# Kernel optimization log

Measured on AMD Instinct MI355X. Metric: run time of the kernel, lower is better.

## Reference

```python
import jax, jax.numpy as jnp
import numpy as np

N, D, OUT, E, K = 65536, 256, 256, 8, 2  # tokens, input_dim, output_dim, num_experts, top-k


def setup_inputs() -> dict:
    key = jax.random.key(0)
    k1, k2, k3, k4 = jax.random.split(key, 4)
    x = jax.random.normal(k1, (N, D), dtype=jnp.float32)
    # xavier_normal-like init for the gate
    w_gate = jax.random.normal(k2, (D, E), dtype=jnp.float32) * np.float32(np.sqrt(2.0 / (D + E)))
    # PWLayer params stacked over experts: bias init zeros, weight std 0.02
    expert_bias = jax.random.normal(k3, (E, D), dtype=jnp.float32) * 0.01
    expert_weight = jax.random.normal(k4, (E, OUT, D), dtype=jnp.float32) * 0.02
    return {"x": x, "w_gate": w_gate, "expert_bias": expert_bias, "expert_weight": expert_weight}


def reference(x, w_gate, expert_bias, expert_weight):
    # --- noisy_top_k_gating (eval mode: clean logits only) ---
    logits = x @ w_gate                                   # [N, E]
    top_v, top_i = jax.lax.top_k(logits, K)               # [N, K]
    sparse_logits = jnp.full_like(logits, -jnp.inf)
    rows = jnp.arange(logits.shape[0])[:, None]           # [N, 1]
    sparse_logits = sparse_logits.at[rows, top_i].set(top_v)
    gates = jax.nn.softmax(sparse_logits, axis=-1)        # [N, E], zeros off the top-k
    # --- dense all-expert PWLayer pass: (x - bias_e) @ W_e^T ---
    centered = x[:, None, :] - expert_bias[None, :, :]    # [N, E, D]
    expert_stack = jnp.einsum('ned,eod->neo', centered, expert_weight)  # [N, E, OUT]
    # --- gated combine ---
    return jnp.einsum('ne,neo->no', gates, expert_stack)  # [N, OUT]
```

## Files before the change

kernel.cpp:

```cpp
#include <hip/hip_runtime.h>
#include <hip/hip_bf16.h>
#include <math.h>

#define N_TOK 65536
#define DIM   256
#define NEXP  8

using frag_ab = __attribute__((ext_vector_type(8))) short;
using frag_cd = __attribute__((ext_vector_type(4))) float;

__device__ __forceinline__ unsigned short f2bf(float f) {
  unsigned u = __float_as_uint(f);
  u += 0x7FFFu + ((u >> 16) & 1u);
  return (unsigned short)(u >> 16);
}

__device__ __forceinline__ void gl2lds16(const unsigned short* g, unsigned short* l) {
  __builtin_amdgcn_global_load_lds(
      (const __attribute__((address_space(1))) void*)g,
      (__attribute__((address_space(3))) void*)l, 16, 0, 0);
}


__global__ __launch_bounds__(256) void k_prep(
    const float* __restrict__ w,
    const float* __restrict__ bias,
    unsigned short* __restrict__ Wb,
    float* __restrict__ c,
    int* __restrict__ meta) {
  int tid = threadIdx.x;
  int wid = (blockIdx.x * 256 + tid) >> 6;
  int lane = tid & 63;
  int e = wid >> 8, o = wid & 255;
  const float* wr = w + (size_t)(e * 256 + o) * DIM + lane * 4;
  float4 wv = *(const float4*)wr;
  const float* br = bias + e * DIM + lane * 4;
  float4 bv = *(const float4*)br;
  float s = wv.x * bv.x + wv.y * bv.y + wv.z * bv.z + wv.w * bv.w;
  #pragma unroll
  for (int m = 1; m < 64; m <<= 1) s += __shfl_xor(s, m, 64);
  if (lane == 0) c[e * 256 + o] = s;
  ushort4 h; h.x = f2bf(wv.x); h.y = f2bf(wv.y); h.z = f2bf(wv.z); h.w = f2bf(wv.w);
  *(ushort4*)(Wb + (size_t)e * 65536 + (size_t)(lane >> 1) * 2048 + o * 8 + (lane & 1) * 4) = h;
  if (blockIdx.x == 0 && tid < 192) meta[tid] = 0;
}

__global__ __launch_bounds__(256) void k_gating(
    const float* __restrict__ x,
    const float* __restrict__ wg,
    unsigned short* __restrict__ xb,
    int* __restrict__ routeE,
    float* __restrict__ routeG,
    int* __restrict__ meta) {
  __shared__ double swg[DIM * NEXP];
  __shared__ float  chunk[128 * 33];
  __shared__ double sPar[128 * NEXP];
  __shared__ int    hcnt[64];
  int tid = threadIdx.x;
  int tok0 = blockIdx.x * 128;
  int sub = tid >> 7, tk = tid & 127;

  for (int i = tid; i < DIM * NEXP; i += 256) swg[i] = (double)wg[i];
  if (tid < 64) hcnt[tid] = 0;

  double p[NEXP];
  #pragma unroll
  for (int e = 0; e < NEXP; e++) p[e] = 0.0;

  for (int dc = 0; dc < 8; dc++) {
    __syncthreads();
    #pragma unroll
    for (int i = 0; i < 4; i++) {
      int f = i * 256 + tid;
      int r = f >> 3, c4 = (f & 7) * 4;
      const float4 v = *(const float4*)(x + (size_t)(tok0 + r) * DIM + dc * 32 + c4);
      ushort4 h; h.x = f2bf(v.x); h.y = f2bf(v.y); h.z = f2bf(v.z); h.w = f2bf(v.w);
      *(ushort4*)(xb + (size_t)(tok0 + r) * DIM + dc * 32 + c4) = h;
      float* dst = &chunk[r * 33 + c4];
      dst[0] = v.x; dst[1] = v.y; dst[2] = v.z; dst[3] = v.w;
    }
    __syncthreads();
    if ((dc >> 2) == sub) {
      #pragma unroll 8
      for (int cc = 0; cc < 32; cc++) {
        double xv = (double)chunk[tk * 33 + cc];
        const double* wrow = &swg[(dc * 32 + cc) * NEXP];
        #pragma unroll
        for (int e = 0; e < NEXP; e++) p[e] += xv * wrow[e];
      }
    }
  }

  if (sub == 1) {
    #pragma unroll
    for (int e = 0; e < NEXP; e++) sPar[tk * NEXP + e] = p[e];
  }
  __syncthreads();
  if (sub == 0) {
    #pragma unroll
    for (int e = 0; e < NEXP; e++) p[e] += sPar[tk * NEXP + e];

    int i1 = 0; double v1 = p[0];
    #pragma unroll
    for (int e = 1; e < NEXP; e++) { if (p[e] > v1) { v1 = p[e]; i1 = e; } }
    int i2 = -1; double v2 = -1e300;
    #pragma unroll
    for (int e = 0; e < NEXP; e++) { if (e != i1 && p[e] > v2) { v2 = p[e]; i2 = e; } }
    double t = exp(v2 - v1);
    float g1 = (float)(1.0 / (1.0 + t));
    float g2 = 1.0f - g1;

    int n = tok0 + tk;
    routeE[n] = i1 | (i2 << 8);
    *(float2*)(routeG + 2 * (size_t)n) = make_float2(g1, g2);
    int a = i1 < i2 ? i1 : i2, b = i1 < i2 ? i2 : i1;
    atomicAdd(&hcnt[a * 8 + b], 1);
  }
  __syncthreads();
  if (tid < 64) atomicAdd(&meta[tid], hcnt[tid]);
}

__global__ void k_scan(int* __restrict__ meta) {
  if (threadIdx.x == 0) {
    int run = 0;
    for (int p = 0; p < 64; p++) {
      meta[64 + p] = run; meta[128 + p] = run;
      run += ((meta[p] + 127) >> 7) << 7;
    }
  }
}

__global__ __launch_bounds__(1024) void k_scatter(
    const int* __restrict__ routeE, const float* __restrict__ routeG,
    int* __restrict__ meta,
    int* __restrict__ srcTok, float* __restrict__ srcGA, float* __restrict__ srcGB) {
  __shared__ int cnt[64], bse[64];
  int tid = threadIdx.x;
  if (tid < 64) cnt[tid] = 0;
  __syncthreads();
  int n = blockIdx.x * 1024 + tid;
  int ep = routeE[n];
  int e1 = ep & 255, e2 = ep >> 8;
  float2 g = *(const float2*)(routeG + 2 * (size_t)n);
  int a = e1 < e2 ? e1 : e2, b = e1 < e2 ? e2 : e1;
  float ga = e1 < e2 ? g.x : g.y;
  float gb = e1 < e2 ? g.y : g.x;
  int pid = a * 8 + b;
  int r = atomicAdd(&cnt[pid], 1);
  __syncthreads();
  if (tid < 64) bse[tid] = atomicAdd(&meta[128 + tid], cnt[tid]);
  __syncthreads();
  int p = bse[pid] + r;
  srcTok[p] = n; srcGA[p] = ga; srcGB[p] = gb;
}

__global__ __launch_bounds__(512, 2) void k_gemm_pair(
    const unsigned short* __restrict__ xb,
    const unsigned short* __restrict__ Wb,
    const int* __restrict__ meta,
    const int* __restrict__ srcTok,
    const float* __restrict__ srcGA, const float* __restrict__ srcGB,
    const float* __restrict__ c,
    float* __restrict__ out) {
  __shared__ unsigned short sA[4][128 * 64];
  __shared__ int   sTok[128];
  __shared__ float sGAs[128], sGBs[128];
  __shared__ float sCorA[256], sCorB[256];
  int tid = threadIdx.x;

  int rem = blockIdx.x, pid = 0, ne = 0;
  for (pid = 0; pid < 64; pid++) {
    ne = meta[pid];
    int tiles = (ne + 127) >> 7;
    if (rem < tiles) break;
    rem -= tiles;
  }
  if (pid == 64) return;
  int ea = pid >> 3, eb = pid & 7;
  int mt = rem;
  int slot0 = meta[64 + pid] + mt * 128;

  if (tid < 128) {
    int idx = mt * 128 + tid;
    bool v = idx < ne;
    sTok[tid]  = v ? srcTok[slot0 + tid] : 0;
    sGAs[tid]  = v ? srcGA[slot0 + tid] : 0.f;
    sGBs[tid]  = v ? srcGB[slot0 + tid] : 1.f;
  } else if (tid < 192) {
    ((float4*)sCorA)[tid - 128] = ((const float4*)(c + ea * 256))[tid - 128];
  } else if (tid < 256) {
    ((float4*)sCorB)[tid - 192] = ((const float4*)(c + eb * 256))[tid - 192];
  }
  __syncthreads();

  int w = tid >> 6, lane = tid & 63;
  int lrow = lane >> 3, lchk = lane & 7;

  #pragma unroll
  for (int q = 0; q < 2; q++) {
    int r0 = w * 16 + q * 8;
    int r  = r0 + lrow;
    int cc = (lchk - r) & 7;
    const unsigned short* src = xb + (size_t)sTok[r] * 256 + cc * 8;
    #pragma unroll
    for (int kk = 0; kk < 4; kk++)
      gl2lds16(src + kk * 64, &sA[kk][r0 * 64]);
  }
  __syncthreads();

  int wm = w & 1, wn = w >> 1;
  int lr = lane & 15, lk = lane >> 4;
  int offA[2][4];
  #pragma unroll
  for (int ks = 0; ks < 2; ks++)
    #pragma unroll
    for (int i = 0; i < 4; i++) {
      int ra = wm * 64 + i * 16 + lr;
      offA[ks][i] = ra * 64 + ((ks * 4 + lk + ra) & 7) * 8;
    }

  const unsigned short* bBaseA =
      Wb + (size_t)ea * 65536 + (size_t)lk * 2048 + (wn * 64 + lr) * 8;
  const unsigned short* bBaseB =
      Wb + (size_t)eb * 65536 + (size_t)lk * 2048 + (wn * 64 + lr) * 8;

  frag_cd acc[4][4];
  #pragma unroll
  for (int i = 0; i < 4; i++)
    #pragma unroll
    for (int j = 0; j < 4; j++)
      acc[i][j] = (frag_cd){0.f, 0.f, 0.f, 0.f};

#define PHASE(BB) do {                                                      \
    _Pragma("unroll")                                                       \
    for (int kk = 0; kk < 4; kk++) {                                        \
      _Pragma("unroll")                                                     \
      for (int ks = 0; ks < 2; ks++) {                                      \
        frag_ab av[4], bv[4];                                               \
        _Pragma("unroll")                                                   \
        for (int j = 0; j < 4; j++)                                         \
          bv[j] = *(const frag_ab*)((BB) + kk * 16384 + ks * 8192 + j * 128); \
        _Pragma("unroll")                                                   \
        for (int i = 0; i < 4; i++) av[i] = *(const frag_ab*)(&sA[kk][0] + offA[ks][i]); \
        _Pragma("unroll")                                                   \
        for (int i = 0; i < 4; i++)                                         \
          _Pragma("unroll")                                                 \
          for (int j = 0; j < 4; j++)                                       \
            acc[i][j] = __builtin_amdgcn_mfma_f32_16x16x32_bf16(av[i], bv[j], acc[i][j], 0, 0, 0); \
      }                                                                     \
    }                                                                       \
  } while (0)

  PHASE(bBaseA);

  #pragma unroll
  for (int i = 0; i < 4; i++)
    #pragma unroll
    for (int rr = 0; rr < 4; rr++) {
      int m = wm * 64 + i * 16 + lk * 4 + rr;
      float ratio = sGAs[m] / sGBs[m];
      #pragma unroll
      for (int j = 0; j < 4; j++) acc[i][j][rr] *= ratio;
    }

  PHASE(bBaseB);

#undef PHASE

  #pragma unroll
  for (int i = 0; i < 4; i++) {
    #pragma unroll
    for (int rr = 0; rr < 4; rr++) {
      int m = wm * 64 + i * 16 + lk * 4 + rr;
      if (mt * 128 + m < ne) {
        int tokn = sTok[m];
        float sa = sGAs[m], sb = sGBs[m];
        float* orow = out + (size_t)tokn * 256;
        #pragma unroll
        for (int j = 0; j < 4; j++) {
          int col = wn * 64 + j * 16 + lr;
          orow[col] = sb * acc[i][j][rr] - (sa * sCorA[col] + sb * sCorB[col]);
        }
      }
    }
  }
}

extern "C" void kernel_launch(void* const* d_in, const int* in_sizes, int n_in,
                              void* d_out, int out_size, void* d_ws, size_t ws_size,
                              hipStream_t stream) {
  const float* x    = (const float*)d_in[0];
  const float* wg   = (const float*)d_in[1];
  const float* bias = (const float*)d_in[2];
  const float* w    = (const float*)d_in[3];
  float* out = (float*)d_out;
  char* ws = (char*)d_ws;

  unsigned short* xb = (unsigned short*)(ws);
  unsigned short* Wb = (unsigned short*)(ws + 33554432);
  float* c           = (float*)(ws + 34603008);
  int* meta          = (int*)(ws + 34611200);
  int* routeE        = (int*)(ws + 34612224);
  float* routeG      = (float*)(ws + 34874368);
  int* srcTok        = (int*)(ws + 35398656);
  float* srcGA       = (float*)(ws + 35678720);
  float* srcGB       = (float*)(ws + 35958784);

  hipLaunchKernelGGL(k_prep,      dim3(512),  dim3(256),  0, stream, w, bias, Wb, c, meta);
  hipLaunchKernelGGL(k_gating,    dim3(512),  dim3(256),  0, stream, x, wg, xb, routeE, routeG, meta);
  hipLaunchKernelGGL(k_scan,      dim3(1),    dim3(64),   0, stream, meta);
  hipLaunchKernelGGL(k_scatter,   dim3(64),   dim3(1024), 0, stream, routeE, routeG, meta,
                     srcTok, srcGA, srcGB);
  hipLaunchKernelGGL(k_gemm_pair, dim3(544),  dim3(512),  0, stream, xb, Wb,
                     meta, srcTok, srcGA, srcGB, c, out);
}
```

Before: 197.6 us.

## Split gating dot product across 4 lanes per token and prefetch x chunks

```diff
diff --git a/kernel.cpp b/kernel.cpp
--- a/kernel.cpp
+++ b/kernel.cpp
@@ -53,12 +53,11 @@
     float* __restrict__ routeG,
     int* __restrict__ meta) {
   __shared__ double swg[DIM * NEXP];
-  __shared__ float  chunk[128 * 33];
-  __shared__ double sPar[128 * NEXP];
+  __shared__ float  chunk[64 * 35];
   __shared__ int    hcnt[64];
   int tid = threadIdx.x;
-  int tok0 = blockIdx.x * 128;
-  int sub = tid >> 7, tk = tid & 127;
+  int tok0 = blockIdx.x * 64;
+  int tk = tid >> 2, sub = tid & 3;
 
   for (int i = tid; i < DIM * NEXP; i += 256) swg[i] = (double)wg[i];
   if (tid < 64) hcnt[tid] = 0;
@@ -67,46 +66,61 @@
   #pragma unroll
   for (int e = 0; e < NEXP; e++) p[e] = 0.0;
 
+  int f0 = tid, f1 = 256 + tid;
+  int r0 = f0 >> 3, c40 = (f0 & 7) * 4;
+  int r1 = f1 >> 3, c41 = (f1 & 7) * 4;
+  const float* xs0 = x + (size_t)(tok0 + r0) * DIM + c40;
+  const float* xs1 = x + (size_t)(tok0 + r1) * DIM + c41;
+  unsigned short* xd0 = xb + (size_t)(tok0 + r0) * DIM + c40;
+  unsigned short* xd1 = xb + (size_t)(tok0 + r1) * DIM + c41;
+
+  float4 v0 = *(const float4*)(xs0);
+  float4 v1 = *(const float4*)(xs1);
+
   for (int dc = 0; dc < 8; dc++) {
     __syncthreads();
-    #pragma unroll
-    for (int i = 0; i < 4; i++) {
-      int f = i * 256 + tid;
-      int r = f >> 3, c4 = (f & 7) * 4;
-      const float4 v = *(const float4*)(x + (size_t)(tok0 + r) * DIM + dc * 32 + c4);
-      ushort4 h; h.x = f2bf(v.x); h.y = f2bf(v.y); h.z = f2bf(v.z); h.w = f2bf(v.w);
-      *(ushort4*)(xb + (size_t)(tok0 + r) * DIM + dc * 32 + c4) = h;
-      float* dst = &chunk[r * 33 + c4];
-      dst[0] = v.x; dst[1] = v.y; dst[2] = v.z; dst[3] = v.w;
+    {
+      ushort4 h0; h0.x = f2bf(v0.x); h0.y = f2bf(v0.y); h0.z = f2bf(v0.z); h0.w = f2bf(v0.w);
+      ushort4 h1; h1.x = f2bf(v1.x); h1.y = f2bf(v1.y); h1.z = f2bf(v1.z); h1.w = f2bf(v1.w);
+      *(ushort4*)(xd0 + dc * 32) = h0;
+      *(ushort4*)(xd1 + dc * 32) = h1;
+      float* d0 = &chunk[r0 * 35 + c40];
+      d0[0] = v0.x; d0[1] = v0.y; d0[2] = v0.z; d0[3] = v0.w;
+      float* d1 = &chunk[r1 * 35 + c41];
+      d1[0] = v1.x; d1[1] = v1.y; d1[2] = v1.z; d1[3] = v1.w;
+    }
+    float4 n0 = make_float4(0.f, 0.f, 0.f, 0.f);
+    float4 n1 = make_float4(0.f, 0.f, 0.f, 0.f);
+    if (dc < 7) {
+      n0 = *(const float4*)(xs0 + (dc + 1) * 32);
+      n1 = *(const float4*)(xs1 + (dc + 1) * 32);
     }
     __syncthreads();
-    if ((dc >> 2) == sub) {
-      #pragma unroll 8
-      for (int cc = 0; cc < 32; cc++) {
-        double xv = (double)chunk[tk * 33 + cc];
-        const double* wrow = &swg[(dc * 32 + cc) * NEXP];
-        #pragma unroll
-        for (int e = 0; e < NEXP; e++) p[e] += xv * wrow[e];
-      }
-    }
-  }
-
-  if (sub == 1) {
-    #pragma unroll
-    for (int e = 0; e < NEXP; e++) sPar[tk * NEXP + e] = p[e];
-  }
-  __syncthreads();
+    #pragma unroll
+    for (int c8 = 0; c8 < 8; c8++) {
+      int cc = c8 * 4 + sub;
+      double xv = (double)chunk[tk * 35 + cc];
+      const double* wrow = &swg[(dc * 32 + cc) * NEXP];
+      #pragma unroll
+      for (int e = 0; e < NEXP; e++) p[e] += xv * wrow[e];
+    }
+    v0 = n0; v1 = n1;
+  }
+
+  #pragma unroll
+  for (int e = 0; e < NEXP; e++) {
+    p[e] += __shfl_xor(p[e], 1, 64);
+    p[e] += __shfl_xor(p[e], 2, 64);
+  }
+
   if (sub == 0) {
-    #pragma unroll
-    for (int e = 0; e < NEXP; e++) p[e] += sPar[tk * NEXP + e];
-
-    int i1 = 0; double v1 = p[0];
-    #pragma unroll
-    for (int e = 1; e < NEXP; e++) { if (p[e] > v1) { v1 = p[e]; i1 = e; } }
-    int i2 = -1; double v2 = -1e300;
-    #pragma unroll
-    for (int e = 0; e < NEXP; e++) { if (e != i1 && p[e] > v2) { v2 = p[e]; i2 = e; } }
-    double t = exp(v2 - v1);
+    int i1 = 0; double v1d = p[0];
+    #pragma unroll
+    for (int e = 1; e < NEXP; e++) { if (p[e] > v1d) { v1d = p[e]; i1 = e; } }
+    int i2 = -1; double v2d = -1e300;
+    #pragma unroll
+    for (int e = 0; e < NEXP; e++) { if (e != i1 && p[e] > v2d) { v2d = p[e]; i2 = e; } }
+    double t = exp(v2d - v1d);
     float g1 = (float)(1.0 / (1.0 + t));
     float g2 = 1.0f - g1;
 
@@ -307,7 +321,7 @@
   float* srcGB       = (float*)(ws + 35958784);
 
   hipLaunchKernelGGL(k_prep,      dim3(512),  dim3(256),  0, stream, w, bias, Wb, c, meta);
-  hipLaunchKernelGGL(k_gating,    dim3(512),  dim3(256),  0, stream, x, wg, xb, routeE, routeG, meta);
+  hipLaunchKernelGGL(k_gating,    dim3(1024), dim3(256),  0, stream, x, wg, xb, routeE, routeG, meta);
   hipLaunchKernelGGL(k_scan,      dim3(1),    dim3(64),   0, stream, meta);
   hipLaunchKernelGGL(k_scatter,   dim3(64),   dim3(1024), 0, stream, routeE, routeG, meta,
                      srcTok, srcGA, srcGB);
```

Result: faster. 180.4 us (-8.7%).
